# Kernel tuning notes

Hardware: AMD Instinct MI355X
Metric: run time of the kernel (lower is better)

## Reference

```python
import jax, jax.numpy as jnp
import numpy as np

N_NODES = 16384
N_EDGES = 131072
EDGE_DIM = 16
IN_CH = 32
OUT_CH = 32
HID_EDGE = 64
MLP_HID = 64  # int(32 * 2.0)
OUT_FINAL = 10
N_GRAPHS = 64
BN_EPS = 1e-5


def setup_inputs() -> dict:
    key = jax.random.key(0)
    ks = jax.random.split(key, 20)
    s = lambda *sh: 1.0 / np.sqrt(sh[0])
    inp = {
        'x': jax.random.normal(ks[0], (N_NODES, IN_CH), jnp.float32),
        'edge_attr': jax.random.normal(ks[1], (N_EDGES, EDGE_DIM), jnp.float32),
        'edge_index': jax.random.randint(ks[2], (2, N_EDGES), 0, N_NODES, jnp.int64),
        'batch': jnp.sort(jax.random.randint(ks[3], (N_NODES,), 0, N_GRAPHS, jnp.int64)),
    }
    # layer 0: edge MLP (EDGE_DIM->HID_EDGE->IN_CH*OUT_CH), root, bias, BN affine
    inp['w1_0'] = jax.random.normal(ks[4], (EDGE_DIM, HID_EDGE), jnp.float32) * s(EDGE_DIM)
    inp['b1_0'] = jnp.zeros((HID_EDGE,), jnp.float32)
    inp['w2_0'] = jax.random.normal(ks[5], (HID_EDGE, IN_CH * OUT_CH), jnp.float32) * s(HID_EDGE)
    inp['b2_0'] = jnp.zeros((IN_CH * OUT_CH,), jnp.float32)
    inp['root_0'] = jax.random.normal(ks[6], (IN_CH, OUT_CH), jnp.float32) * s(IN_CH)
    inp['bias_0'] = jnp.zeros((OUT_CH,), jnp.float32)
    inp['gamma_0'] = jnp.ones((OUT_CH,), jnp.float32)
    inp['beta_0'] = jnp.zeros((OUT_CH,), jnp.float32)
    # layer 1: edge MLP (EDGE_DIM->HID_EDGE->OUT_CH*OUT_CH)
    inp['w1_1'] = jax.random.normal(ks[7], (EDGE_DIM, HID_EDGE), jnp.float32) * s(EDGE_DIM)
    inp['b1_1'] = jnp.zeros((HID_EDGE,), jnp.float32)
    inp['w2_1'] = jax.random.normal(ks[8], (HID_EDGE, OUT_CH * OUT_CH), jnp.float32) * s(HID_EDGE)
    inp['b2_1'] = jnp.zeros((OUT_CH * OUT_CH,), jnp.float32)
    inp['root_1'] = jax.random.normal(ks[9], (OUT_CH, OUT_CH), jnp.float32) * s(OUT_CH)
    inp['bias_1'] = jnp.zeros((OUT_CH,), jnp.float32)
    inp['gamma_1'] = jnp.ones((OUT_CH,), jnp.float32)
    inp['beta_1'] = jnp.zeros((OUT_CH,), jnp.float32)
    # final MLP (dropout is identity in eval / deterministic reference)
    inp['mlp_w1'] = jax.random.normal(ks[10], (OUT_CH, MLP_HID), jnp.float32) * s(OUT_CH)
    inp['mlp_b1'] = jnp.zeros((MLP_HID,), jnp.float32)
    inp['mlp_w2'] = jax.random.normal(ks[11], (MLP_HID, OUT_FINAL), jnp.float32) * s(MLP_HID)
    inp['mlp_b2'] = jnp.zeros((OUT_FINAL,), jnp.float32)
    return inp


def _nnconv(x, src, dst, edge_attr, w1, b1, w2, b2, root, bias, out_ch):
    # per-edge weight matrices from the edge MLP: [E, in, out]
    h = jax.nn.relu(edge_attr @ w1 + b1)
    W = (h @ w2 + b2).reshape(-1, x.shape[1], out_ch)
    msg = jnp.einsum('ei,eio->eo', x[src], W)  # gather + per-edge matmul
    agg = jax.ops.segment_sum(msg, dst, num_segments=N_NODES)
    cnt = jax.ops.segment_sum(jnp.ones((dst.shape[0], 1), x.dtype), dst, num_segments=N_NODES)
    agg = agg / jnp.maximum(cnt, 1.0)  # scatter-mean (zero-degree nodes -> 0)
    return agg + x @ root + bias


def _bn(x, gamma, beta):
    m = jnp.mean(x, axis=0)
    v = jnp.var(x, axis=0)
    return (x - m) * jax.lax.rsqrt(v + BN_EPS) * gamma + beta


def reference(x, edge_attr, edge_index, batch,
              w1_0, b1_0, w2_0, b2_0, root_0, bias_0, gamma_0, beta_0,
              w1_1, b1_1, w2_1, b2_1, root_1, bias_1, gamma_1, beta_1,
              mlp_w1, mlp_b1, mlp_w2, mlp_b2):
    src, dst = edge_index[0], edge_index[1]
    h = _nnconv(x, src, dst, edge_attr, w1_0, b1_0, w2_0, b2_0, root_0, bias_0, OUT_CH)
    h = jax.nn.relu(_bn(h, gamma_0, beta_0))
    h = _nnconv(h, src, dst, edge_attr, w1_1, b1_1, w2_1, b2_1, root_1, bias_1, OUT_CH)
    h = jax.nn.relu(_bn(h, gamma_1, beta_1))
    # global mean pool over graphs
    pooled = jax.ops.segment_sum(h, batch, num_segments=N_GRAPHS)
    gcnt = jax.ops.segment_sum(jnp.ones((h.shape[0], 1), h.dtype), batch, num_segments=N_GRAPHS)
    pooled = pooled / jnp.maximum(gcnt, 1.0)
    logits = jax.nn.relu(pooled @ mlp_w1 + mlp_b1) @ mlp_w2 + mlp_b2
    return logits
```

## Files before the change

kernel.cpp:

```cpp
#include <hip/hip_runtime.h>
#include <hip/hip_bf16.h>

#define NN 16384
#define NE 131072
#define NG 64
#define EPB 128

typedef unsigned short u16;
typedef unsigned int u32;
typedef __attribute__((ext_vector_type(8))) short short8;
typedef __attribute__((ext_vector_type(4))) float f32x4;
typedef __attribute__((ext_vector_type(2))) float f32x2;

__device__ __forceinline__ float bf2f(u16 u) {
    u32 x = ((u32)u) << 16;
    return __builtin_bit_cast(float, x);
}
__device__ __forceinline__ u16 f2bf(float f) {
    u32 u = __builtin_bit_cast(u32, f);
    u = u + 0x7fffu + ((u >> 16) & 1u);
    return (u16)(u >> 16);
}
__device__ __forceinline__ u32 pk2bf(float a, float b) {
    return (u32)f2bf(a) | ((u32)f2bf(b) << 16);
}
#if __has_builtin(__builtin_amdgcn_cvt_pk_bf16_f32)
__device__ __forceinline__ u32 pk2bf_fast(float a, float b) {
    auto v = __builtin_amdgcn_cvt_pk_bf16_f32(a, b);
    static_assert(sizeof(v) == 4, "cvt_pk_bf16 size");
    return __builtin_bit_cast(u32, v);
}
#else
__device__ __forceinline__ u32 pk2bf_fast(float a, float b) {
    u32 ua = __builtin_bit_cast(u32, a) + 0x8000u;
    u32 ub = __builtin_bit_cast(u32, b) + 0x8000u;
    return __builtin_amdgcn_perm(ub, ua, 0x07060302u);
}
#endif
__device__ __forceinline__ float loadF(const void* p, int i, bool bf) {
    return bf ? bf2f(((const u16*)p)[i]) : ((const float*)p)[i];
}
__device__ __forceinline__ int loadI(const void* p, int i, bool i64) {
    return i64 ? (int)((const long long*)p)[i] : ((const int*)p)[i];
}
__device__ __forceinline__ bool det_bf(const void* g0) {
    return ((const u16*)g0)[0] == 0x3F80u;
}
__device__ __forceinline__ bool det_i64(const void* eidx) {
    const u32* u = (const u32*)eidx;
    return (u[1] | u[3] | u[5] | u[7]) == 0u;
}

__global__ __launch_bounds__(256) void k_prep(const void* w2a, const void* b2a,
                                              const void* w2b, const void* b2b,
                                              const void* w1a, const void* w1b,
                                              u16* bp0, u16* bp1, u16* w1p0, u16* w1p1,
                                              const void* eidx, float* cnt, const void* g0) {
    const bool bf = det_bf(g0);
    int id = blockIdx.x * 256 + threadIdx.x;
    if (id < 2 * 66560) {
        int l = id / 66560, v = id % 66560;
        int j = v & 7, lane = (v >> 3) & 63, nt = (v >> 9) & 1, t = v >> 10;
        int kk = (lane >> 4) * 8 + j;
        int n = (lane & 15) + 16 * nt;
        const void* w2 = l ? w2b : w2a;
        const void* b2 = l ? b2b : b2a;
        float val = (t < 64) ? loadF(w2, t * 1024 + kk * 32 + n, bf)
                             : loadF(b2, kk * 32 + n, bf);
        (l ? bp1 : bp0)[v] = f2bf(val);
    } else if (id < 2 * 66560 + 2 * 2048) {
        int v = id - 2 * 66560;
        int l = v >> 11; v &= 2047;
        int j = v & 7, lane = (v >> 3) & 63, nt = v >> 9;
        int k = (lane >> 4) * 8 + j;
        int n = nt * 16 + (lane & 15);
        const void* w1 = l ? w1b : w1a;
        float val = (k < 16) ? loadF(w1, k * 64 + n, bf) : 0.f;
        (l ? w1p1 : w1p0)[v] = f2bf(val);
    } else {
        const bool i64 = det_i64(eidx);
        int e = id - (2 * 66560 + 2 * 2048);
        int d = loadI(eidx, NE + e, i64);
        atomicAdd(&cnt[d], 1.0f);
    }
}

#define HSTR 72
__global__ __launch_bounds__(256, 4) void k_edge(const void* ea, const u16* w1p, const void* b1,
                                                 const void* xv, int layer1,
                                                 const float* sSp, const float* sQp,
                                                 const void* gammap, const void* betap,
                                                 const void* eidx, const u16* Bpack,
                                                 float* agg, const void* g0) {
    const bool bf = det_bf(g0);
    const bool i64 = det_i64(eidx);
    __shared__ __align__(16) u16 hl[EPB * HSTR];
    __shared__ __align__(16) float bnS[32], bnB[32];
    const int tid = threadIdx.x;
    const int e0 = blockIdx.x * EPB;
    const int lane = tid & 63;
    const int w = tid >> 6;
    const int q = lane >> 4;
    const int m = lane & 15;
    const int wbl = w * 32;
    const int wb = e0 + wbl;

    if (layer1 && tid < 32) {
        float s = 0.f, qq = 0.f;
#pragma unroll
        for (int p = 0; p < 16; p++) { s += sSp[p * 32 + tid]; qq += sQp[p * 32 + tid]; }
        float mn = s * (1.0f / 16384.0f);
        float var = qq * (1.0f / 16384.0f) - mn * mn;
        float inv = rsqrtf(var + 1e-5f);
        float g = loadF(gammap, tid, bf), b = loadF(betap, tid, bf);
        bnS[tid] = inv * g;
        bnB[tid] = b - mn * inv * g;
    }

    {
        short8 Ah[2];
#pragma unroll
        for (int e2 = 0; e2 < 2; e2++) {
            int eg = wb + e2 * 16 + m;
            uint4 av = make_uint4(0u, 0u, 0u, 0u);
            if (bf) {
                uint4 t = *(const uint4*)((const char*)ea + (size_t)eg * 32 + (q & 1) * 16);
                if (q < 2) av = t;
            } else {
                const float4* p = (const float4*)((const char*)ea + (size_t)eg * 64 + (q & 1) * 32);
                float4 a = p[0], b = p[1];
                if (q < 2) av = make_uint4(pk2bf_fast(a.x, a.y), pk2bf_fast(a.z, a.w),
                                           pk2bf_fast(b.x, b.y), pk2bf_fast(b.z, b.w));
            }
            Ah[e2] = __builtin_bit_cast(short8, av);
        }
#pragma unroll
        for (int nt = 0; nt < 4; nt++) {
            uint4 bw = *(const uint4*)&w1p[(nt * 64 + lane) * 8];
            short8 Bf = __builtin_bit_cast(short8, bw);
            float bb = loadF(b1, nt * 16 + m, bf);
#pragma unroll
            for (int e2 = 0; e2 < 2; e2++) {
                f32x4 c = __builtin_amdgcn_mfma_f32_16x16x32_bf16(
                    Ah[e2], Bf, f32x4{0.f, 0.f, 0.f, 0.f}, 0, 0, 0);
                int rbase = (wbl + e2 * 16 + q * 4) * HSTR + nt * 16 + m;
#pragma unroll
                for (int r = 0; r < 4; r++) {
                    u32 pkd = pk2bf_fast(fmaxf(c[r] + bb, 0.f), 0.f);
                    hl[rbase + r * HSTR] = (u16)pkd;
                }
            }
        }
    }

    float4 ga[2], gb[2];
#pragma unroll
    for (int mt = 0; mt < 2; mt++) {
        int s = loadI(eidx, wb + mt * 16 + m, i64);
        if (layer1 || !bf) {
            const float4* xp = (const float4*)xv + (size_t)s * 8 + q * 2;
            ga[mt] = xp[0]; gb[mt] = xp[1];
        } else {
            const uint4* xp = (const uint4*)((const char*)xv + (size_t)s * 64 + q * 16);
            uint4 a = *xp;
            ga[mt] = make_float4(bf2f((u16)(a.x & 0xffff)), bf2f((u16)(a.x >> 16)),
                                 bf2f((u16)(a.y & 0xffff)), bf2f((u16)(a.y >> 16)));
            gb[mt] = make_float4(bf2f((u16)(a.z & 0xffff)), bf2f((u16)(a.z >> 16)),
                                 bf2f((u16)(a.w & 0xffff)), bf2f((u16)(a.w >> 16)));
        }
    }

    const uint4* bp4 = (const uint4*)Bpack;
    uint4 pb[4][2];
#pragma unroll
    for (int d = 0; d < 4; d++) {
        pb[d][0] = bp4[(d * 2 + 0) * 64 + lane];
        pb[d][1] = bp4[(d * 2 + 1) * 64 + lane];
    }

    __syncthreads();

    f32x2 xr2[2][4];
    if (layer1) {
        float4 s0 = *(const float4*)&bnS[q * 8], s1 = *(const float4*)&bnS[q * 8 + 4];
        float4 h0 = *(const float4*)&bnB[q * 8], h1 = *(const float4*)&bnB[q * 8 + 4];
#pragma unroll
        for (int mt = 0; mt < 2; mt++) {
            xr2[mt][0] = f32x2{fmaxf(ga[mt].x * s0.x + h0.x, 0.f), fmaxf(ga[mt].y * s0.y + h0.y, 0.f)};
            xr2[mt][1] = f32x2{fmaxf(ga[mt].z * s0.z + h0.z, 0.f), fmaxf(ga[mt].w * s0.w + h0.w, 0.f)};
            xr2[mt][2] = f32x2{fmaxf(gb[mt].x * s1.x + h1.x, 0.f), fmaxf(gb[mt].y * s1.y + h1.y, 0.f)};
            xr2[mt][3] = f32x2{fmaxf(gb[mt].z * s1.z + h1.z, 0.f), fmaxf(gb[mt].w * s1.w + h1.w, 0.f)};
        }
    } else {
#pragma unroll
        for (int mt = 0; mt < 2; mt++) {
            xr2[mt][0] = f32x2{ga[mt].x, ga[mt].y};
            xr2[mt][1] = f32x2{ga[mt].z, ga[mt].w};
            xr2[mt][2] = f32x2{gb[mt].x, gb[mt].y};
            xr2[mt][3] = f32x2{gb[mt].z, gb[mt].w};
        }
    }

    f32x4 acc[2][2];
#pragma unroll
    for (int mt = 0; mt < 2; mt++) {
        acc[mt][0] = f32x4{0.f, 0.f, 0.f, 0.f};
        acc[mt][1] = f32x4{0.f, 0.f, 0.f, 0.f};
    }
    int rowb[2];
#pragma unroll
    for (int mt = 0; mt < 2; mt++) rowb[mt] = (wbl + mt * 16 + m) * HSTR;

    for (int tc = 0; tc < 8; tc++) {
        uint4 hb[2];
        hb[0] = *(const uint4*)&hl[rowb[0] + tc * 8];
        hb[1] = *(const uint4*)&hl[rowb[1] + tc * 8];
#pragma unroll
        for (int tj = 0; tj < 8; tj++) {
            int t = tc * 8 + tj;
            int slot = tj & 3;
            uint4 bu0 = pb[slot][0], bu1 = pb[slot][1];
            int tn = t + 4; if (tn > 64) tn = 64;
            pb[slot][0] = bp4[(tn * 2 + 0) * 64 + lane];
            pb[slot][1] = bp4[(tn * 2 + 1) * 64 + lane];
            short8 B0 = __builtin_bit_cast(short8, bu0);
            short8 B1 = __builtin_bit_cast(short8, bu1);
#pragma unroll
            for (int mt = 0; mt < 2; mt++) {
                u32 wd = ((const u32*)&hb[mt])[tj >> 1];
                u32 hbits = (tj & 1) ? (wd & 0xFFFF0000u) : (wd << 16);
                float hs = __builtin_bit_cast(float, hbits);
                f32x2 h2 = {hs, hs};
                f32x2 p0 = h2 * xr2[mt][0];
                f32x2 p1 = h2 * xr2[mt][1];
                f32x2 p2 = h2 * xr2[mt][2];
                f32x2 p3 = h2 * xr2[mt][3];
                uint4 au = make_uint4(pk2bf_fast(p0.x, p0.y), pk2bf_fast(p1.x, p1.y),
                                      pk2bf_fast(p2.x, p2.y), pk2bf_fast(p3.x, p3.y));
                short8 A = __builtin_bit_cast(short8, au);
                acc[mt][0] = __builtin_amdgcn_mfma_f32_16x16x32_bf16(A, B0, acc[mt][0], 0, 0, 0);
                acc[mt][1] = __builtin_amdgcn_mfma_f32_16x16x32_bf16(A, B1, acc[mt][1], 0, 0, 0);
            }
        }
    }
    {
        short8 B0 = __builtin_bit_cast(short8, pb[0][0]);
        short8 B1 = __builtin_bit_cast(short8, pb[0][1]);
#pragma unroll
        for (int mt = 0; mt < 2; mt++) {
            uint4 au = make_uint4(pk2bf_fast(xr2[mt][0].x, xr2[mt][0].y),
                                  pk2bf_fast(xr2[mt][1].x, xr2[mt][1].y),
                                  pk2bf_fast(xr2[mt][2].x, xr2[mt][2].y),
                                  pk2bf_fast(xr2[mt][3].x, xr2[mt][3].y));
            short8 A = __builtin_bit_cast(short8, au);
            acc[mt][0] = __builtin_amdgcn_mfma_f32_16x16x32_bf16(A, B0, acc[mt][0], 0, 0, 0);
            acc[mt][1] = __builtin_amdgcn_mfma_f32_16x16x32_bf16(A, B1, acc[mt][1], 0, 0, 0);
        }
    }

#pragma unroll
    for (int mt = 0; mt < 2; mt++) {
        int eb = wb + mt * 16 + q * 4;
#pragma unroll
        for (int r = 0; r < 4; r++) {
            int dst = loadI(eidx, NE + eb + r, i64);
            float* ap = agg + (size_t)dst * 32 + m;
            atomicAdd(ap, acc[mt][0][r]);
            atomicAdd(ap + 16, acc[mt][1][r]);
        }
    }
}

__global__ __launch_bounds__(256) void k_node(float* agg, const float* cnt,
                                              const void* xv, int layer1,
                                              const float* sSp, const float* sQp,
                                              const void* gammap, const void* betap,
                                              const void* root, const void* bias,
                                              float* hpre, float* sS, float* sQ,
                                              const void* g0) {
    const bool bf = det_bf(g0);
    const int tid = threadIdx.x;
    const int v = blockIdx.x * 8 + (tid >> 5);
    const int o = tid & 31;
    __shared__ float bnS[32], bnB[32];
    if (layer1) {
        if (tid < 32) {
            float s = 0.f, qq = 0.f;
#pragma unroll
            for (int p = 0; p < 16; p++) { s += sSp[p * 32 + tid]; qq += sQp[p * 32 + tid]; }
            float mn = s * (1.0f / 16384.0f);
            float var = qq * (1.0f / 16384.0f) - mn * mn;
            float inv = rsqrtf(var + 1e-5f);
            float g = loadF(gammap, tid, bf), b = loadF(betap, tid, bf);
            bnS[tid] = inv * g;
            bnB[tid] = b - mn * inv * g;
        }
        __syncthreads();
    }
    float xrow[32];
    if (layer1) {
        const float* x = (const float*)xv + (size_t)v * 32;
#pragma unroll
        for (int i = 0; i < 32; i++) xrow[i] = fmaxf(x[i] * bnS[i] + bnB[i], 0.f);
    } else if (!bf) {
        const float* x = (const float*)xv + (size_t)v * 32;
#pragma unroll
        for (int i = 0; i < 32; i++) xrow[i] = x[i];
    } else {
        const u16* x = (const u16*)xv + (size_t)v * 32;
#pragma unroll
        for (int i = 0; i < 32; i++) xrow[i] = bf2f(x[i]);
    }
    float a;
    if (bf) {
        const u16* R = (const u16*)root;
        a = bf2f(((const u16*)bias)[o]);
#pragma unroll
        for (int i = 0; i < 32; i++) a += xrow[i] * bf2f(R[i * 32 + o]);
    } else {
        const float* R = (const float*)root;
        a = ((const float*)bias)[o];
#pragma unroll
        for (int i = 0; i < 32; i++) a += xrow[i] * R[i * 32 + o];
    }
    float av = agg[(size_t)v * 32 + o];
    agg[(size_t)v * 32 + o] = 0.f;
    float pre = av / fmaxf(cnt[v], 1.0f) + a;
    hpre[(size_t)v * 32 + o] = pre;

    __shared__ float lS[256], lQ[256];
    lS[tid] = pre;
    lQ[tid] = pre * pre;
    __syncthreads();
#pragma unroll
    for (int off = 128; off >= 32; off >>= 1) {
        if (tid < off) { lS[tid] += lS[tid + off]; lQ[tid] += lQ[tid + off]; }
        __syncthreads();
    }
    if (tid < 32) {
        int slot = (blockIdx.x & 15) * 32 + tid;
        atomicAdd(&sS[slot], lS[tid]);
        atomicAdd(&sQ[slot], lQ[tid]);
    }
}

__global__ __launch_bounds__(256) void k_bnpool(const float* hpre, const float* sS, const float* sQ,
                                                const void* gamma, const void* beta,
                                                const void* batch, float* pooled, float* gcnt,
                                                const void* eidx, const void* g0) {
    const bool bf = det_bf(g0);
    const bool i64 = det_i64(eidx);
    const int tid = threadIdx.x;
    const int o = tid & 31;
    const int c = tid >> 5;
    float s = 0.f, qq = 0.f;
#pragma unroll
    for (int p = 0; p < 16; p++) { s += sS[p * 32 + o]; qq += sQ[p * 32 + o]; }
    float mn = s * (1.0f / 16384.0f);
    float var = qq * (1.0f / 16384.0f) - mn * mn;
    float inv = rsqrtf(var + 1e-5f);
    float gg = loadF(gamma, o, bf), bb = loadF(beta, o, bf);

    const int base = blockIdx.x * 256 + c;
    float acc = 0.f, cacc = 0.f;
    int curg = -1;
#pragma unroll 4
    for (int j = 0; j < 32; j++) {
        int v = base + j * 8;
        int g = loadI(batch, v, i64);
        float y = fmaxf((hpre[(size_t)v * 32 + o] - mn) * inv * gg + bb, 0.f);
        if (g != curg) {
            if (curg >= 0) {
                atomicAdd(&pooled[curg * 32 + o], acc);
                if (o == 0) atomicAdd(&gcnt[curg], cacc);
            }
            acc = 0.f; cacc = 0.f; curg = g;
        }
        acc += y; cacc += 1.f;
    }
    if (curg >= 0) {
        atomicAdd(&pooled[curg * 32 + o], acc);
        if (o == 0) atomicAdd(&gcnt[curg], cacc);
    }
}

__global__ __launch_bounds__(64) void k_final(const float* pooled, const float* gcnt,
                        const void* w1, const void* b1, const void* w2, const void* b2,
                        void* out, const void* g0) {
    const bool bf = det_bf(g0);
    const int g = blockIdx.x;
    const int j = threadIdx.x;
    float inv = 1.0f / fmaxf(gcnt[g], 1.0f);
    float a = loadF(b1, j, bf);
#pragma unroll
    for (int i = 0; i < 32; i++) {
        float p = pooled[g * 32 + i] * inv;
        a += p * loadF(w1, i * 64 + j, bf);
    }
    a = fmaxf(a, 0.f);
    float lg[10];
#pragma unroll
    for (int c = 0; c < 10; c++) lg[c] = a * loadF(w2, j * 10 + c, bf);
#pragma unroll
    for (int off = 32; off >= 1; off >>= 1) {
#pragma unroll
        for (int c = 0; c < 10; c++) lg[c] += __shfl_down(lg[c], off, 64);
    }
    if (j == 0) {
        if (bf) {
            u16* op = (u16*)out;
#pragma unroll
            for (int c = 0; c < 10; c++) op[g * 10 + c] = f2bf(lg[c] + loadF(b2, c, bf));
        } else {
            float* op = (float*)out;
#pragma unroll
            for (int c = 0; c < 10; c++) op[g * 10 + c] = lg[c] + loadF(b2, c, bf);
        }
    }
}

extern "C" void kernel_launch(void* const* d_in, const int* in_sizes, int n_in,
                              void* d_out, int out_size, void* d_ws, size_t ws_size,
                              hipStream_t stream) {
    char* ws = (char*)d_ws;
    u16* bp0  = (u16*)(ws + 256);
    u16* bp1  = (u16*)(ws + 256 + 133120);
    u16* w1p0 = (u16*)(ws + 266496);
    u16* w1p1 = (u16*)(ws + 270592);
    char* zbase = ws + 274688;
    float* agg    = (float*)(zbase);
    float* cnt    = (float*)(zbase + 2097152);
    float* sS0    = (float*)(zbase + 2162688);
    float* sQ0    = (float*)(zbase + 2164736);
    float* sS1    = (float*)(zbase + 2166784);
    float* sQ1    = (float*)(zbase + 2168832);
    float* pooled = (float*)(zbase + 2170880);
    float* gcnt   = (float*)(zbase + 2179072);
    const size_t zsize = 2179328;
    float* hpre0 = (float*)(ws + 274688 + 2179328);
    float* hpre1 = (float*)(ws + 274688 + 2179328 + 2097152);

    const void* x     = d_in[0];
    const void* ea    = d_in[1];
    const void* eidx  = d_in[2];
    const void* batch = d_in[3];
    const void* g0    = d_in[10];

    (void)hipMemsetAsync(zbase, 0, zsize, stream);
    k_prep<<<1048, 256, 0, stream>>>(d_in[6], d_in[7], d_in[14], d_in[15],
                                     d_in[4], d_in[12],
                                     bp0, bp1, w1p0, w1p1, eidx, cnt, g0);

    k_edge<<<NE / EPB, 256, 0, stream>>>(ea, w1p0, d_in[5], x, 0,
                                         nullptr, nullptr, nullptr, nullptr,
                                         eidx, bp0, agg, g0);
    k_node<<<NN / 8, 256, 0, stream>>>(agg, cnt, x, 0,
                                       nullptr, nullptr, nullptr, nullptr,
                                       d_in[8], d_in[9], hpre0, sS0, sQ0, g0);

    k_edge<<<NE / EPB, 256, 0, stream>>>(ea, w1p1, d_in[13], hpre0, 1,
                                         sS0, sQ0, d_in[10], d_in[11],
                                         eidx, bp1, agg, g0);
    k_node<<<NN / 8, 256, 0, stream>>>(agg, cnt, hpre0, 1,
                                       sS0, sQ0, d_in[10], d_in[11],
                                       d_in[16], d_in[17], hpre1, sS1, sQ1, g0);

    k_bnpool<<<NN / 256, 256, 0, stream>>>(hpre1, sS1, sQ1, d_in[18], d_in[19], batch,
                                           pooled, gcnt, eidx, g0);
    k_final<<<NG, 64, 0, stream>>>(pooled, gcnt, d_in[20], d_in[21], d_in[22], d_in[23], d_out, g0);
}
```

Measured before the change: 217.7 us.

## Switch edge message GEMM to fp16 packed math and stage weights via LDS

Replaces the bf16 MFMA path in the edge kernel with fp16: the hidden activations, node features and packed second-layer weights are stored as fp16. The per-element products are formed with packed f16 multiplies instead of fp32 multiplies followed by bf16 conversion. Weight chunks are now staged into a double-buffered LDS region with global_load_lds instead of per-lane register prefetch from global memory. This cuts conversion ALU work and register pressure, at the cost of one block-wide barrier per chunk, extra LDS, and fp16 range/precision risk (round-toward-zero packing, possible overflow).

New measurement: 212.9 us. 2.2% less time.

```diff
diff --git a/kernel.cpp b/kernel.cpp
--- a/kernel.cpp
+++ b/kernel.cpp
@@ -11,6 +11,10 @@
 typedef __attribute__((ext_vector_type(8))) short short8;
 typedef __attribute__((ext_vector_type(4))) float f32x4;
 typedef __attribute__((ext_vector_type(2))) float f32x2;
+typedef __attribute__((ext_vector_type(8))) _Float16 f16x8;
+typedef __attribute__((ext_vector_type(2))) _Float16 f16x2;
+typedef __attribute__((address_space(1))) const unsigned int gu32;
+typedef __attribute__((address_space(3))) unsigned int lu32;
 
 __device__ __forceinline__ float bf2f(u16 u) {
     u32 x = ((u32)u) << 16;
@@ -21,8 +25,14 @@
     u = u + 0x7fffu + ((u >> 16) & 1u);
     return (u16)(u >> 16);
 }
-__device__ __forceinline__ u32 pk2bf(float a, float b) {
-    return (u32)f2bf(a) | ((u32)f2bf(b) << 16);
+__device__ __forceinline__ u16 f2h(float f) {
+    _Float16 h = (_Float16)f;
+    return __builtin_bit_cast(u16, h);
+}
+__device__ __forceinline__ f16x2 pkrtz(float a, float b) {
+    auto v = __builtin_amdgcn_cvt_pkrtz(a, b);
+    static_assert(sizeof(v) == 4, "pkrtz size");
+    return __builtin_bit_cast(f16x2, v);
 }
 #if __has_builtin(__builtin_amdgcn_cvt_pk_bf16_f32)
 __device__ __forceinline__ u32 pk2bf_fast(float a, float b) {
@@ -67,7 +77,7 @@
         const void* b2 = l ? b2b : b2a;
         float val = (t < 64) ? loadF(w2, t * 1024 + kk * 32 + n, bf)
                              : loadF(b2, kk * 32 + n, bf);
-        (l ? bp1 : bp0)[v] = f2bf(val);
+        (l ? bp1 : bp0)[v] = f2h(val);
     } else if (id < 2 * 66560 + 2 * 2048) {
         int v = id - 2 * 66560;
         int l = v >> 11; v &= 2047;
@@ -85,6 +95,13 @@
     }
 }
 
+__device__ __forceinline__ void stage_chunk(const u16* Bpack, u16* lds, int cc, int w, int lane) {
+    const char* src = (const char*)Bpack + (size_t)cc * 8192 + (size_t)(w * 1024 + lane * 16);
+    char* dst = (char*)lds + w * 1024;
+    __builtin_amdgcn_global_load_lds((gu32*)src, (lu32*)dst, 16, 0, 0);
+    __builtin_amdgcn_global_load_lds((gu32*)(src + 4096), (lu32*)(dst + 4096), 16, 0, 0);
+}
+
 #define HSTR 72
 __global__ __launch_bounds__(256, 4) void k_edge(const void* ea, const u16* w1p, const void* b1,
                                                  const void* xv, int layer1,
@@ -95,6 +112,7 @@
     const bool bf = det_bf(g0);
     const bool i64 = det_i64(eidx);
     __shared__ __align__(16) u16 hl[EPB * HSTR];
+    __shared__ __align__(16) u16 Bls[2][4096];
     __shared__ __align__(16) float bnS[32], bnB[32];
     const int tid = threadIdx.x;
     const int e0 = blockIdx.x * EPB;
@@ -104,6 +122,9 @@
     const int m = lane & 15;
     const int wbl = w * 32;
     const int wb = e0 + wbl;
+
+    stage_chunk(Bpack, Bls[0], 0, w, lane);
+    stage_chunk(Bpack, Bls[1], 1, w, lane);
 
     if (layer1 && tid < 32) {
         float s = 0.f, qq = 0.f;
@@ -146,8 +167,8 @@
                 int rbase = (wbl + e2 * 16 + q * 4) * HSTR + nt * 16 + m;
 #pragma unroll
                 for (int r = 0; r < 4; r++) {
-                    u32 pkd = pk2bf_fast(fmaxf(c[r] + bb, 0.f), 0.f);
-                    hl[rbase + r * HSTR] = (u16)pkd;
+                    _Float16 hv = (_Float16)fmaxf(c[r] + bb, 0.f);
+                    hl[rbase + r * HSTR] = __builtin_bit_cast(u16, hv);
                 }
             }
         }
@@ -170,34 +191,30 @@
         }
     }
 
-    const uint4* bp4 = (const uint4*)Bpack;
-    uint4 pb[4][2];
-#pragma unroll
-    for (int d = 0; d < 4; d++) {
-        pb[d][0] = bp4[(d * 2 + 0) * 64 + lane];
-        pb[d][1] = bp4[(d * 2 + 1) * 64 + lane];
-    }
-
     __syncthreads();
 
-    f32x2 xr2[2][4];
+    f16x2 xh[2][4];
     if (layer1) {
         float4 s0 = *(const float4*)&bnS[q * 8], s1 = *(const float4*)&bnS[q * 8 + 4];
         float4 h0 = *(const float4*)&bnB[q * 8], h1 = *(const float4*)&bnB[q * 8 + 4];
 #pragma unroll
         for (int mt = 0; mt < 2; mt++) {
-            xr2[mt][0] = f32x2{fmaxf(ga[mt].x * s0.x + h0.x, 0.f), fmaxf(ga[mt].y * s0.y + h0.y, 0.f)};
-            xr2[mt][1] = f32x2{fmaxf(ga[mt].z * s0.z + h0.z, 0.f), fmaxf(ga[mt].w * s0.w + h0.w, 0.f)};
-            xr2[mt][2] = f32x2{fmaxf(gb[mt].x * s1.x + h1.x, 0.f), fmaxf(gb[mt].y * s1.y + h1.y, 0.f)};
-            xr2[mt][3] = f32x2{fmaxf(gb[mt].z * s1.z + h1.z, 0.f), fmaxf(gb[mt].w * s1.w + h1.w, 0.f)};
+            xh[mt][0] = pkrtz(fmaxf(ga[mt].x * s0.x + h0.x, 0.f),
+                              fmaxf(ga[mt].y * s0.y + h0.y, 0.f));
+            xh[mt][1] = pkrtz(fmaxf(ga[mt].z * s0.z + h0.z, 0.f),
+                              fmaxf(ga[mt].w * s0.w + h0.w, 0.f));
+            xh[mt][2] = pkrtz(fmaxf(gb[mt].x * s1.x + h1.x, 0.f),
+                              fmaxf(gb[mt].y * s1.y + h1.y, 0.f));
+            xh[mt][3] = pkrtz(fmaxf(gb[mt].z * s1.z + h1.z, 0.f),
+                              fmaxf(gb[mt].w * s1.w + h1.w, 0.f));
         }
     } else {
 #pragma unroll
         for (int mt = 0; mt < 2; mt++) {
-            xr2[mt][0] = f32x2{ga[mt].x, ga[mt].y};
-            xr2[mt][1] = f32x2{ga[mt].z, ga[mt].w};
-            xr2[mt][2] = f32x2{gb[mt].x, gb[mt].y};
-            xr2[mt][3] = f32x2{gb[mt].z, gb[mt].w};
+            xh[mt][0] = pkrtz(ga[mt].x, ga[mt].y);
+            xh[mt][1] = pkrtz(ga[mt].z, ga[mt].w);
+            xh[mt][2] = pkrtz(gb[mt].x, gb[mt].y);
+            xh[mt][3] = pkrtz(gb[mt].z, gb[mt].w);
         }
     }
 
@@ -211,50 +228,50 @@
 #pragma unroll
     for (int mt = 0; mt < 2; mt++) rowb[mt] = (wbl + mt * 16 + m) * HSTR;
 
-    for (int tc = 0; tc < 8; tc++) {
-        uint4 hb[2];
-        hb[0] = *(const uint4*)&hl[rowb[0] + tc * 8];
-        hb[1] = *(const uint4*)&hl[rowb[1] + tc * 8];
-#pragma unroll
-        for (int tj = 0; tj < 8; tj++) {
-            int t = tc * 8 + tj;
-            int slot = tj & 3;
-            uint4 bu0 = pb[slot][0], bu1 = pb[slot][1];
-            int tn = t + 4; if (tn > 64) tn = 64;
-            pb[slot][0] = bp4[(tn * 2 + 0) * 64 + lane];
-            pb[slot][1] = bp4[(tn * 2 + 1) * 64 + lane];
-            short8 B0 = __builtin_bit_cast(short8, bu0);
-            short8 B1 = __builtin_bit_cast(short8, bu1);
+    for (int cc = 0; cc < 16; cc++) {
+        uint2 hw[2];
+        hw[0] = *(const uint2*)&hl[rowb[0] + cc * 4];
+        hw[1] = *(const uint2*)&hl[rowb[1] + cc * 4];
+        const u16* Bb = &Bls[cc & 1][lane * 8];
+#pragma unroll
+        for (int tt = 0; tt < 4; tt++) {
+            uint4 bu0 = *(const uint4*)(Bb + (tt * 2 + 0) * 512);
+            uint4 bu1 = *(const uint4*)(Bb + (tt * 2 + 1) * 512);
+            f16x8 B0 = __builtin_bit_cast(f16x8, bu0);
+            f16x8 B1 = __builtin_bit_cast(f16x8, bu1);
+            const u32 sel = (tt & 1) ? 0x03020302u : 0x01000100u;
 #pragma unroll
             for (int mt = 0; mt < 2; mt++) {
-                u32 wd = ((const u32*)&hb[mt])[tj >> 1];
-                u32 hbits = (tj & 1) ? (wd & 0xFFFF0000u) : (wd << 16);
-                float hs = __builtin_bit_cast(float, hbits);
-                f32x2 h2 = {hs, hs};
-                f32x2 p0 = h2 * xr2[mt][0];
-                f32x2 p1 = h2 * xr2[mt][1];
-                f32x2 p2 = h2 * xr2[mt][2];
-                f32x2 p3 = h2 * xr2[mt][3];
-                uint4 au = make_uint4(pk2bf_fast(p0.x, p0.y), pk2bf_fast(p1.x, p1.y),
-                                      pk2bf_fast(p2.x, p2.y), pk2bf_fast(p3.x, p3.y));
-                short8 A = __builtin_bit_cast(short8, au);
-                acc[mt][0] = __builtin_amdgcn_mfma_f32_16x16x32_bf16(A, B0, acc[mt][0], 0, 0, 0);
-                acc[mt][1] = __builtin_amdgcn_mfma_f32_16x16x32_bf16(A, B1, acc[mt][1], 0, 0, 0);
+                u32 wd = (tt & 2) ? hw[mt].y : hw[mt].x;
+                u32 hh = __builtin_amdgcn_perm(wd, wd, sel);
+                f16x2 h2 = __builtin_bit_cast(f16x2, hh);
+                f16x2 p0 = h2 * xh[mt][0];
+                f16x2 p1 = h2 * xh[mt][1];
+                f16x2 p2 = h2 * xh[mt][2];
+                f16x2 p3 = h2 * xh[mt][3];
+                uint4 au = make_uint4(__builtin_bit_cast(u32, p0), __builtin_bit_cast(u32, p1),
+                                      __builtin_bit_cast(u32, p2), __builtin_bit_cast(u32, p3));
+                f16x8 A = __builtin_bit_cast(f16x8, au);
+                acc[mt][0] = __builtin_amdgcn_mfma_f32_16x16x32_f16(A, B0, acc[mt][0], 0, 0, 0);
+                acc[mt][1] = __builtin_amdgcn_mfma_f32_16x16x32_f16(A, B1, acc[mt][1], 0, 0, 0);
             }
         }
+        __syncthreads();
+        if (cc < 15) stage_chunk(Bpack, Bls[cc & 1], cc + 2, w, lane);
     }
     {
-        short8 B0 = __builtin_bit_cast(short8, pb[0][0]);
-        short8 B1 = __builtin_bit_cast(short8, pb[0][1]);
+        const u16* Bb = &Bls[0][lane * 8];
+        uint4 bu0 = *(const uint4*)(Bb + 0);
+        uint4 bu1 = *(const uint4*)(Bb + 512);
+        f16x8 B0 = __builtin_bit_cast(f16x8, bu0);
+        f16x8 B1 = __builtin_bit_cast(f16x8, bu1);
 #pragma unroll
         for (int mt = 0; mt < 2; mt++) {
-            uint4 au = make_uint4(pk2bf_fast(xr2[mt][0].x, xr2[mt][0].y),
-                                  pk2bf_fast(xr2[mt][1].x, xr2[mt][1].y),
-                                  pk2bf_fast(xr2[mt][2].x, xr2[mt][2].y),
-                                  pk2bf_fast(xr2[mt][3].x, xr2[mt][3].y));
-            short8 A = __builtin_bit_cast(short8, au);
-            acc[mt][0] = __builtin_amdgcn_mfma_f32_16x16x32_bf16(A, B0, acc[mt][0], 0, 0, 0);
-            acc[mt][1] = __builtin_amdgcn_mfma_f32_16x16x32_bf16(A, B1, acc[mt][1], 0, 0, 0);
+            uint4 au = make_uint4(__builtin_bit_cast(u32, xh[mt][0]), __builtin_bit_cast(u32, xh[mt][1]),
+                                  __builtin_bit_cast(u32, xh[mt][2]), __builtin_bit_cast(u32, xh[mt][3]));
+            f16x8 A = __builtin_bit_cast(f16x8, au);
+            acc[mt][0] = __builtin_amdgcn_mfma_f32_16x16x32_f16(A, B0, acc[mt][0], 0, 0, 0);
+            acc[mt][1] = __builtin_amdgcn_mfma_f32_16x16x32_f16(A, B1, acc[mt][1], 0, 0, 0);
         }
     }
 
```
